# Performance work log

Hardware: AMD Instinct MI355X
Metric: run time of the kernel (lower is better)

## Reference

```python
import jax, jax.numpy as jnp
import numpy as np

HEADS = 8
DIM_HEAD = 64
SCALE = DIM_HEAD ** -0.5


def setup_inputs() -> dict:
    key = jax.random.key(0)
    ks = jax.random.split(key, 7)
    B, N, Dq = 2, 4096, 512
    M, Dc = 4096, 768
    inner = HEADS * DIM_HEAD  # 512
    x = jax.random.normal(ks[0], (B, N, Dq), dtype=jnp.float32)
    context = jax.random.normal(ks[1], (B, M, Dc), dtype=jnp.float32)
    # weights stored [in, out] (torch Linear weight transposed)
    Wq = jax.random.normal(ks[2], (Dq, inner), dtype=jnp.float32) * (Dq ** -0.5)
    Wk = jax.random.normal(ks[3], (Dc, inner), dtype=jnp.float32) * (Dc ** -0.5)
    Wv = jax.random.normal(ks[4], (Dc, inner), dtype=jnp.float32) * (Dc ** -0.5)
    Wo = jax.random.normal(ks[5], (inner, Dq), dtype=jnp.float32) * (inner ** -0.5)
    bo = jax.random.normal(ks[6], (Dq,), dtype=jnp.float32) * 0.01
    return {"x": x, "context": context, "Wq": Wq, "Wk": Wk, "Wv": Wv, "Wo": Wo, "bo": bo}


def reference(x, context, Wq, Wk, Wv, Wo, bo):
    B, N, _ = x.shape
    M = context.shape[1]
    h, d = HEADS, DIM_HEAD
    q = (x @ Wq).reshape(B, N, h, d)                      # b n h d
    k = ((context @ Wk) * SCALE).reshape(B, M, h, d)      # scale applied to k, as in source
    v = (context @ Wv).reshape(B, M, h, d)
    scores = jnp.einsum('bnhd,bmhd->bhnm', q, k)          # full QK^T
    attn = jax.nn.softmax(scores, axis=-1)
    out = jnp.einsum('bhnm,bmhd->bnhd', attn, v).reshape(B, N, h * d)
    return out @ Wo + bo  # dropout p=0.0 -> identity
```

## Files before the change

### kernel.cpp

```cpp
#include <hip/hip_runtime.h>

typedef unsigned short u16;
typedef __attribute__((ext_vector_type(4))) unsigned short u16x4;
typedef __attribute__((ext_vector_type(8))) unsigned short u16x8;
typedef __attribute__((ext_vector_type(8))) short s16x8;
typedef __attribute__((ext_vector_type(4))) float f32x4;
typedef __attribute__((ext_vector_type(16))) float f32x16;
typedef __attribute__((ext_vector_type(4))) unsigned int u32x4;

#define LOG2E 1.4426950408889634f

__device__ __forceinline__ u16 f2bf(float f) {
    return __builtin_bit_cast(unsigned short, static_cast<__bf16>(f));
}

__device__ __forceinline__ float bf2f(u16 v) {
    return __builtin_bit_cast(float, (unsigned)v << 16);
}

__device__ __forceinline__ float fexp2(float x) {
#if __has_builtin(__builtin_amdgcn_exp2f)
    return __builtin_amdgcn_exp2f(x);
#else
    return exp2f(x);
#endif
}

__device__ __forceinline__ s16x8 ld_frag(const u16* p) {
    return __builtin_bit_cast(s16x8, *reinterpret_cast<const u16x8*>(p));
}

__device__ __forceinline__ f32x4 mfma16(s16x8 a, s16x8 b, f32x4 c) {
    return __builtin_amdgcn_mfma_f32_16x16x32_bf16(a, b, c, 0, 0, 0);
}

__device__ __forceinline__ f32x16 mfma32(s16x8 a, s16x8 b, f32x16 c) {
    return __builtin_amdgcn_mfma_f32_32x32x16_bf16(a, b, c, 0, 0, 0);
}

__device__ __forceinline__ unsigned cvt_pk_bf16(float lo, float hi2) {
    unsigned r;
    asm("v_cvt_pk_bf16_f32 %0, %1, %2" : "=v"(r) : "v"(lo), "v"(hi2));
    return r;
}

__device__ __forceinline__ void plane32_swap(unsigned& x, unsigned& y) {
#if __has_builtin(__builtin_amdgcn_permlane32_swap)
    auto r = __builtin_amdgcn_permlane32_swap(x, y, false, false);
    x = r[0];
    y = r[1];
#else
    asm("v_permlane32_swap_b32 %0, %1" : "+v"(x), "+v"(y));
#endif
}

__device__ __forceinline__ void async16(const u16* g, u16* lds) {
    __builtin_amdgcn_global_load_lds(
        (__attribute__((address_space(1))) void*)const_cast<u16*>(g),
        (__attribute__((address_space(3))) void*)lds, 16, 0, 0);
}

__global__ __launch_bounds__(256) void prep_kernel(
    const float* __restrict__ x, const float* __restrict__ ctx, const float* __restrict__ Wq,
    const float* __restrict__ Wk, const float* __restrict__ Wv, const float* __restrict__ Wo,
    u16* __restrict__ xb, u16* __restrict__ cb, u16* __restrict__ Wqt, u16* __restrict__ Wkt,
    u16* __restrict__ Wvt, u16* __restrict__ Wot) {
    __shared__ float t[32][33];
    const int bidx = blockIdx.x;
    const int tid = threadIdx.x;
    if (bidx < 5120) {
        int i = bidx * 256 + tid;
        const float* in;
        u16* out;
        int idx;
        if (i < 524288) {
            in = x; out = xb; idx = i;
        } else {
            in = ctx; out = cb; idx = i - 524288;
        }
        const f32x4* p = (const f32x4*)in + ((size_t)idx << 1);
        f32x4 a = p[0], c = p[1];
        u16x8 v;
        v[0] = f2bf(a[0]); v[1] = f2bf(a[1]); v[2] = f2bf(a[2]); v[3] = f2bf(a[3]);
        v[4] = f2bf(c[0]); v[5] = f2bf(c[1]); v[6] = f2bf(c[2]); v[7] = f2bf(c[3]);
        *((u16x8*)out + idx) = v;
    } else {
        const int zb = bidx - 5120;
        const int z = zb / 384;
        const int rem = zb - z * 384;
        const int kx = rem % 24, ny = rem / 24;
        const float* W;
        u16* Wt;
        int Kd;
        float scale;
        switch (z) {
            case 0: W = Wq; Wt = Wqt; Kd = 512; scale = 1.0f; break;
            case 1: W = Wk; Wt = Wkt; Kd = 768; scale = 0.125f * LOG2E; break;
            case 2: W = Wv; Wt = Wvt; Kd = 768; scale = 1.0f; break;
            default: W = Wo; Wt = Wot; Kd = 512; scale = 1.0f; break;
        }
        const int k0 = kx << 5, n0 = ny << 5;
        if (k0 >= Kd) return;
        const int tx = tid & 31, ty = tid >> 5;
#pragma unroll
        for (int i = 0; i < 32; i += 8)
            t[ty + i][tx] = W[(size_t)(k0 + ty + i) * 512 + n0 + tx] * scale;
        __syncthreads();
#pragma unroll
        for (int i = 0; i < 32; i += 8)
            Wt[(size_t)(n0 + ty + i) * Kd + k0 + tx] = f2bf(t[tx][ty + i]);
    }
}

template <int MODE>
__device__ __forceinline__ void gemm_body(u16* __restrict__ Ab, u16* __restrict__ Bb,
                                          const u16* __restrict__ A, const u16* __restrict__ Bt,
                                          void* __restrict__ Cv, const float* __restrict__ bias,
                                          int K) {
    const int tid = threadIdx.x;
    const int w = tid >> 6, l = tid & 63;
    const int lg = l >> 4, lq = l & 15;
    const int wm = w >> 1, wn = w & 1;
    const int bm = blockIdx.y, bn = blockIdx.x;
    const int KT = K >> 6;

    f32x4 acc[4][4];
#pragma unroll
    for (int i = 0; i < 4; i++)
#pragma unroll
        for (int j = 0; j < 4; j++) acc[i][j] = (f32x4){0.f, 0.f, 0.f, 0.f};

    const u16* Ag0 = A + (size_t)bm * 128 * K;
    const u16* Bg0 = Bt + (size_t)bn * 128 * K;
    const int srow = l >> 3, scol = (l & 7) << 3;

    auto stage = [&](int kt, int buf) {
#pragma unroll
        for (int i = 0; i < 4; i++) {
            const int c = (w << 2) + i;
            const int row = (c << 3) + srow;
            async16(Ag0 + (size_t)row * K + kt * 64 + scol, Ab + (buf << 13) + (c << 9));
            async16(Bg0 + (size_t)row * K + kt * 64 + scol, Bb + (buf << 13) + (c << 9));
        }
    };

    stage(0, 0);
    for (int kt = 0; kt < KT; ++kt) {
        __syncthreads();
        if (kt + 1 < KT) stage(kt + 1, (kt + 1) & 1);
        const u16* As = Ab + ((kt & 1) << 13);
        const u16* Bs = Bb + ((kt & 1) << 13);
#pragma unroll
        for (int s = 0; s < 2; s++) {
            s16x8 af[4], bfr[4];
#pragma unroll
            for (int mt = 0; mt < 4; mt++)
                af[mt] = ld_frag(As + ((wm << 6) + (mt << 4) + lq) * 64 + (s << 5) + (lg << 3));
#pragma unroll
            for (int nt = 0; nt < 4; nt++)
                bfr[nt] = ld_frag(Bs + ((wn << 6) + (nt << 4) + lq) * 64 + (s << 5) + (lg << 3));
#pragma unroll
            for (int mt = 0; mt < 4; mt++)
#pragma unroll
                for (int nt = 0; nt < 4; nt++)
                    acc[mt][nt] = mfma16(af[mt], bfr[nt], acc[mt][nt]);
        }
    }
    const int row0 = bm * 128 + (wm << 6);
    const int col0 = bn * 128 + (wn << 6);
    if constexpr (MODE == 0) {
        u16* C = (u16*)Cv;
#pragma unroll
        for (int mt = 0; mt < 4; mt++)
#pragma unroll
            for (int nt = 0; nt < 4; nt++)
#pragma unroll
                for (int r = 0; r < 4; r++)
                    C[(size_t)(row0 + (mt << 4) + (lg << 2) + r) * 512 + col0 + (nt << 4) + lq] =
                        f2bf(acc[mt][nt][r]);
    } else if constexpr (MODE == 3) {
        float* C = (float*)Cv;
        float bv[4];
#pragma unroll
        for (int nt = 0; nt < 4; nt++) bv[nt] = bias[col0 + (nt << 4) + lq];
#pragma unroll
        for (int mt = 0; mt < 4; mt++)
#pragma unroll
            for (int nt = 0; nt < 4; nt++)
#pragma unroll
                for (int r = 0; r < 4; r++)
                    C[(size_t)(row0 + (mt << 4) + (lg << 2) + r) * 512 + col0 + (nt << 4) + lq] =
                        acc[mt][nt][r] + bv[nt];
    } else {
        __syncthreads();
        u16* Cl = Ab;
#pragma unroll
        for (int mt = 0; mt < 4; mt++)
#pragma unroll
            for (int nt = 0; nt < 4; nt++)
#pragma unroll
                for (int r = 0; r < 4; r++) {
                    const int m = row0 + (mt << 4) + (lg << 2) + r;
                    const int d = (col0 + (nt << 4) + lq) & 63;
                    const int kvl = m & 31;
                    const int tl = (m >> 5) & 3;
                    int op;
                    if constexpr (MODE == 1) {
                        op = ((d >> 4) << 9) + ((kvl + (((d >> 3) & 1) << 5)) << 3) + (d & 7);
                    } else {
                        const int lane = (d & 31) + (((kvl >> 3) & 1) << 5);
                        const int fi = ((kvl >> 4) << 1) + (d >> 5);
                        op = (fi << 9) + (lane << 3) + (kvl & 7);
                    }
                    Cl[(((wn << 2) + tl) << 11) + op] = f2bf(acc[mt][nt][r]);
                }
        __syncthreads();
        u16* C = (u16*)Cv;
#pragma unroll
        for (int c = 0; c < 8; c++) {
            const int bhc = ((bm >> 5) << 3) + (bn << 1) + (c >> 2);
            const int Tc = ((bm & 31) << 2) + (c & 3);
            u16* dst = C + ((size_t)((bhc << 7) + Tc) << 11);
            *(u16x8*)(dst + (tid << 3)) = *(const u16x8*)(Cl + (c << 11) + (tid << 3));
        }
    }
}

__global__ __launch_bounds__(256, 2) void proj_gemm_kernel(
    const u16* __restrict__ xb, const u16* __restrict__ cb, const u16* __restrict__ Wqt,
    const u16* __restrict__ Wkt, const u16* __restrict__ Wvt, u16* __restrict__ Qb,
    u16* __restrict__ Kp, u16* __restrict__ Vp) {
    __shared__ u16 Ab[2][8192];
    __shared__ u16 Bb[2][8192];
    const int z = blockIdx.z;
    if (z == 0)
        gemm_body<0>(&Ab[0][0], &Bb[0][0], xb, Wqt, Qb, nullptr, 512);
    else if (z == 1)
        gemm_body<1>(&Ab[0][0], &Bb[0][0], cb, Wkt, Kp, nullptr, 768);
    else
        gemm_body<2>(&Ab[0][0], &Bb[0][0], cb, Wvt, Vp, nullptr, 768);
}

__global__ __launch_bounds__(256, 2) void out_gemm_kernel(const u16* __restrict__ Ob,
                                                          const u16* __restrict__ Wot,
                                                          float* __restrict__ out,
                                                          const float* __restrict__ bias) {
    __shared__ u16 Ab[2][8192];
    __shared__ u16 Bb[2][8192];
    gemm_body<3>(&Ab[0][0], &Bb[0][0], Ob, Wot, out, bias, 512);
}

__global__ __launch_bounds__(256, 3) void attn_kernel(const u16* __restrict__ Qb,
                                                      const u16* __restrict__ Kp,
                                                      const u16* __restrict__ Vp,
                                                      u16* __restrict__ Opart,
                                                      float* __restrict__ Lpart) {
    __shared__ u16 Kl[2][4096];
    __shared__ u16 Vl[2][4096];
    const int tid = threadIdx.x;
    const int w = tid >> 6, l = tid & 63;
    const int lq = l & 31, hi = l >> 5;
    const int bid = blockIdx.x;
    const int swz = ((bid & 7) << 8) + (bid >> 3);
    const int bh = swz >> 7, qtg = (swz >> 2) & 31, kvseg = swz & 3;
    const int qt = (qtg << 2) + w;
    const int wid = (((bh << 7) + qt) << 2) + kvseg;
    const int b = bh >> 3, h = bh & 7;

    const u16* Qp = Qb + (size_t)(b * 4096 + (qt << 5) + lq) * 512 + (h << 6) + (hi << 3);
    s16x8 qf[4];
#pragma unroll
    for (int s = 0; s < 4; s++) qf[s] = ld_frag(Qp + (s << 4));

    const u16* Kg = Kp + ((size_t)(bh << 7) + (kvseg << 5)) * 2048;
    const u16* Vg = Vp + ((size_t)(bh << 7) + (kvseg << 5)) * 2048;
    const int gsrc = (w << 9) + (l << 3);
    const int ldst = w << 9;
    const int roff = l << 3;

    f32x16 oacc0 = {}, oacc1 = {};
    float rs = 0.f;

    async16(Kg + gsrc, &Kl[0][ldst]);
    async16(Kg + 2048 + gsrc, &Kl[0][2048 + ldst]);
    async16(Vg + gsrc, &Vl[0][ldst]);
    async16(Vg + 2048 + gsrc, &Vl[0][2048 + ldst]);

    auto qk = [&](const u16* Kb_) -> f32x16 {
        f32x16 sacc = {};
        s16x8 fa = ld_frag(Kb_ + roff);
        s16x8 fb = ld_frag(Kb_ + 512 + roff);
        __builtin_amdgcn_s_setprio(1);
        sacc = mfma32(fa, qf[0], sacc);
        fa = ld_frag(Kb_ + 1024 + roff);
        sacc = mfma32(fb, qf[1], sacc);
        fb = ld_frag(Kb_ + 1536 + roff);
        sacc = mfma32(fa, qf[2], sacc);
        sacc = mfma32(fb, qf[3], sacc);
        __builtin_amdgcn_s_setprio(0);
        return sacc;
    };

    auto softmax = [&](f32x16& sacc, s16x8 (&aw)[2]) {
#pragma unroll
        for (int r = 0; r < 16; r++) sacc[r] = fexp2(sacc[r]);
        {
            float t0 = (sacc[0] + sacc[1]) + (sacc[2] + sacc[3]);
            float t1 = (sacc[4] + sacc[5]) + (sacc[6] + sacc[7]);
            float t2 = (sacc[8] + sacc[9]) + (sacc[10] + sacc[11]);
            float t3 = (sacc[12] + sacc[13]) + (sacc[14] + sacc[15]);
            rs += (t0 + t1) + (t2 + t3);
        }
#pragma unroll
        for (int sp = 0; sp < 2; sp++) {
            const int base2 = sp << 3;
            unsigned X1 = cvt_pk_bf16(sacc[base2 + 0], sacc[base2 + 1]);
            unsigned Y1 = cvt_pk_bf16(sacc[base2 + 4], sacc[base2 + 5]);
            unsigned X2 = cvt_pk_bf16(sacc[base2 + 2], sacc[base2 + 3]);
            unsigned Y2 = cvt_pk_bf16(sacc[base2 + 6], sacc[base2 + 7]);
            plane32_swap(X1, Y1);
            plane32_swap(X2, Y2);
            u32x4 wv;
            wv[0] = X1; wv[1] = X2; wv[2] = Y1; wv[3] = Y2;
            aw[sp] = __builtin_bit_cast(s16x8, wv);
        }
    };

    auto pv = [&](const s16x8 (&aw)[2], const u16* Vb_) {
        s16x8 va = ld_frag(Vb_ + roff);
        s16x8 vb = ld_frag(Vb_ + 512 + roff);
        __builtin_amdgcn_s_setprio(1);
        oacc0 = mfma32(aw[0], va, oacc0);
        va = ld_frag(Vb_ + 1024 + roff);
        oacc1 = mfma32(aw[0], vb, oacc1);
        vb = ld_frag(Vb_ + 1536 + roff);
        oacc0 = mfma32(aw[1], va, oacc0);
        oacc1 = mfma32(aw[1], vb, oacc1);
        __builtin_amdgcn_s_setprio(0);
    };

    for (int t = 0; t < 16; ++t) {
        const int buf = t & 1;
        __syncthreads();
        if (t + 1 < 16) {
            const size_t base = (size_t)(t + 1) * 4096;
            const int nb = buf ^ 1;
            async16(Kg + base + gsrc, &Kl[nb][ldst]);
            async16(Kg + base + 2048 + gsrc, &Kl[nb][2048 + ldst]);
            async16(Vg + base + gsrc, &Vl[nb][ldst]);
            async16(Vg + base + 2048 + gsrc, &Vl[nb][2048 + ldst]);
        }
        f32x16 s0 = qk(&Kl[buf][0]);
        f32x16 s1 = qk(&Kl[buf][2048]);
        s16x8 aw0[2], aw1[2];
        softmax(s0, aw0);
        pv(aw0, &Vl[buf][0]);
        softmax(s1, aw1);
        pv(aw1, &Vl[buf][2048]);
    }

    u16* Ow = Opart + ((size_t)wid << 11);
#pragma unroll
    for (int r = 0; r < 16; r++) Ow[(r << 6) + l] = f2bf(oacc0[r]);
#pragma unroll
    for (int r = 0; r < 16; r++) Ow[((16 + r) << 6) + l] = f2bf(oacc1[r]);
    rs += __shfl_xor(rs, 32);
    if (l < 32) Lpart[(wid << 5) + l] = rs;
}

__global__ __launch_bounds__(256) void merge_kernel(const u16* __restrict__ Op,
                                                    const float* __restrict__ Lp,
                                                    u16* __restrict__ Ob) {
    const int g = blockIdx.x * 256 + threadIdx.x;
    const int slot = g >> 8;
    const int idx8 = (g & 255) << 3;
    const int dtr = idx8 >> 6;
    const int r = dtr & 15, dt = dtr >> 4;
    const int lane0 = idx8 & 63;
    const int q = (r & 3) + ((r >> 2) << 3) + ((lane0 >> 5) << 2);
    float lsum = 0.f;
#pragma unroll
    for (int p = 0; p < 4; p++) lsum += Lp[(slot << 7) + (p << 5) + q];
    const float ri = 1.f / lsum;
    float acc[8] = {0.f, 0.f, 0.f, 0.f, 0.f, 0.f, 0.f, 0.f};
#pragma unroll
    for (int p = 0; p < 4; p++) {
        const u16x8 a = *(const u16x8*)(Op + ((size_t)slot << 13) + (p << 11) + idx8);
#pragma unroll
        for (int j = 0; j < 8; j++) acc[j] += bf2f(a[j]);
    }
    u16x8 o;
#pragma unroll
    for (int j = 0; j < 8; j++) o[j] = f2bf(acc[j] * ri);
    const int bh = slot >> 7, qt = slot & 127;
    const int row = ((bh >> 3) << 12) + (qt << 5) + q;
    const int d = (lane0 & 31) + (dt << 5);
    *(u16x8*)(Ob + (size_t)row * 512 + ((bh & 7) << 6) + d) = o;
}

extern "C" void kernel_launch(void* const* d_in, const int* in_sizes, int n_in, void* d_out,
                              int out_size, void* d_ws, size_t ws_size, hipStream_t stream) {
    const float* x = (const float*)d_in[0];
    const float* ctx = (const float*)d_in[1];
    const float* Wq = (const float*)d_in[2];
    const float* Wk = (const float*)d_in[3];
    const float* Wv = (const float*)d_in[4];
    const float* Wo = (const float*)d_in[5];
    const float* bo = (const float*)d_in[6];
    float* out = (float*)d_out;

    char* ws = (char*)d_ws;
    u16* xb  = (u16*)(ws);
    u16* cb  = (u16*)(ws + 8388608);
    u16* Opart   = (u16*)(ws);
    float* Lpart = (float*)(ws + 33554432);
    u16* Qb  = (u16*)(ws + 34603008);
    u16* Ob  = (u16*)(ws + 34603008);
    u16* Kp  = (u16*)(ws + 42991616);
    u16* Vp  = (u16*)(ws + 51380224);
    u16* Wqt = (u16*)(ws + 59768832);
    u16* Wkt = (u16*)(ws + 60293120);
    u16* Wvt = (u16*)(ws + 61079552);
    u16* Wot = (u16*)(ws + 61865984);

    prep_kernel<<<dim3(6656), dim3(256), 0, stream>>>(x, ctx, Wq, Wk, Wv, Wo, xb, cb, Wqt, Wkt,
                                                      Wvt, Wot);
    proj_gemm_kernel<<<dim3(4, 64, 3), dim3(256), 0, stream>>>(xb, cb, Wqt, Wkt, Wvt, Qb, Kp, Vp);
    attn_kernel<<<dim3(2048), dim3(256), 0, stream>>>(Qb, Kp, Vp, Opart, Lpart);
    merge_kernel<<<dim3(2048), dim3(256), 0, stream>>>(Opart, Lpart, Ob);
    out_gemm_kernel<<<dim3(4, 64), dim3(256), 0, stream>>>(Ob, Wot, out, bo);
}
```

Before: 153.9 us.

## Fuse split-KV merge into output projection GEMM and drop setprio in attention

Removes the separate merge kernel and has the output-projection GEMM read the partial attention outputs and row sums directly. It combines the four KV segments, normalises, and writes the bf16 A tile into padded shared memory while the next B tile loads asynchronously. This drops one launch and a round trip of the merged O buffer through memory. The cost is that each of the 4 column blocks re-reads and re-merges the same partials, about four times the partial reads. It also removes the s_setprio hints around the MFMA groups in the attention kernel.

```diff
diff --git a/kernel.cpp b/kernel.cpp
--- a/kernel.cpp
+++ b/kernel.cpp
@@ -178,19 +178,6 @@
                 for (int r = 0; r < 4; r++)
                     C[(size_t)(row0 + (mt << 4) + (lg << 2) + r) * 512 + col0 + (nt << 4) + lq] =
                         f2bf(acc[mt][nt][r]);
-    } else if constexpr (MODE == 3) {
-        float* C = (float*)Cv;
-        float bv[4];
-#pragma unroll
-        for (int nt = 0; nt < 4; nt++) bv[nt] = bias[col0 + (nt << 4) + lq];
-#pragma unroll
-        for (int mt = 0; mt < 4; mt++)
-#pragma unroll
-            for (int nt = 0; nt < 4; nt++)
-#pragma unroll
-                for (int r = 0; r < 4; r++)
-                    C[(size_t)(row0 + (mt << 4) + (lg << 2) + r) * 512 + col0 + (nt << 4) + lq] =
-                        acc[mt][nt][r] + bv[nt];
     } else {
         __syncthreads();
         u16* Cl = Ab;
@@ -241,13 +228,119 @@
         gemm_body<2>(&Ab[0][0], &Bb[0][0], cb, Wvt, Vp, nullptr, 768);
 }
 
-__global__ __launch_bounds__(256, 2) void out_gemm_kernel(const u16* __restrict__ Ob,
-                                                          const u16* __restrict__ Wot,
-                                                          float* __restrict__ out,
-                                                          const float* __restrict__ bias) {
-    __shared__ u16 Ab[2][8192];
+__global__ __launch_bounds__(256, 2) void out_fused_kernel(
+    const u16* __restrict__ Op, const float* __restrict__ Lp, const u16* __restrict__ Wot,
+    float* __restrict__ out, const float* __restrict__ bias) {
+    __shared__ u16 As[2][128 * 72];
     __shared__ u16 Bb[2][8192];
-    gemm_body<3>(&Ab[0][0], &Bb[0][0], Ob, Wot, out, bias, 512);
+    const int tid = threadIdx.x;
+    const int w = tid >> 6, l = tid & 63;
+    const int lg = l >> 4, lq = l & 15;
+    const int wm = w >> 1, wn = w & 1;
+    const int bm = blockIdx.y, bn = blockIdx.x;
+    const int b = bm >> 5, qt0 = (bm & 31) << 2;
+
+    f32x4 acc[4][4];
+#pragma unroll
+    for (int i = 0; i < 4; i++)
+#pragma unroll
+        for (int j = 0; j < 4; j++) acc[i][j] = (f32x4){0.f, 0.f, 0.f, 0.f};
+
+    const u16* Bg0 = Wot + (size_t)bn * 128 * 512;
+    const int srow = l >> 3, scol = (l & 7) << 3;
+
+    auto stageB = [&](int kt, int buf) {
+#pragma unroll
+        for (int i = 0; i < 4; i++) {
+            const int c = (w << 2) + i;
+            const int row = (c << 3) + srow;
+            async16(Bg0 + (size_t)row * 512 + kt * 64 + scol, Bb[buf] + (c << 9));
+        }
+    };
+
+    u16x8 hA[4];
+    auto loadA = [&](int kt) {
+#pragma unroll
+        for (int c = 0; c < 4; c++) {
+            const int qtl = c;
+            const int rem = tid;
+            const int r = (rem >> 3) & 15;
+            const int j = rem & 7;
+            const int q32 = (r & 3) + ((r >> 2) << 3) + ((j >> 2) << 2);
+            const int slot = ((b << 3) + kt) * 128 + qt0 + qtl;
+            const u16* basep = Op + ((size_t)slot << 13) + (rem << 3);
+            float sum[8] = {0.f, 0.f, 0.f, 0.f, 0.f, 0.f, 0.f, 0.f};
+#pragma unroll
+            for (int p = 0; p < 4; p++) {
+                const u16x8 a = *(const u16x8*)(basep + (p << 11));
+#pragma unroll
+                for (int jj = 0; jj < 8; jj++) sum[jj] += bf2f(a[jj]);
+            }
+            const float ls = Lp[(slot << 7) + q32] + Lp[(slot << 7) + 32 + q32] +
+                             Lp[(slot << 7) + 64 + q32] + Lp[(slot << 7) + 96 + q32];
+            const float ri = 1.f / ls;
+            u16x8 hv;
+#pragma unroll
+            for (int jj = 0; jj < 8; jj++) hv[jj] = f2bf(sum[jj] * ri);
+            hA[c] = hv;
+        }
+    };
+    auto writeA = [&](int buf) {
+#pragma unroll
+        for (int c = 0; c < 4; c++) {
+            const int qtl = c;
+            const int rem = tid;
+            const int dt = rem >> 7;
+            const int r = (rem >> 3) & 15;
+            const int j = rem & 7;
+            const int q32 = (r & 3) + ((r >> 2) << 3) + ((j >> 2) << 2);
+            const int d0 = ((j & 3) << 3) + (dt << 5);
+            *(u16x8*)(&As[buf][((qtl << 5) + q32) * 72 + d0]) = hA[c];
+        }
+    };
+
+    stageB(0, 0);
+    loadA(0);
+    writeA(0);
+    for (int kt = 0; kt < 8; ++kt) {
+        __syncthreads();
+        const int buf = kt & 1;
+        if (kt + 1 < 8) {
+            stageB(kt + 1, buf ^ 1);
+            loadA(kt + 1);
+        }
+        const u16* Asb = As[buf];
+        const u16* Bs = Bb[buf];
+#pragma unroll
+        for (int s = 0; s < 2; s++) {
+            s16x8 af[4], bfr[4];
+#pragma unroll
+            for (int mt = 0; mt < 4; mt++)
+                af[mt] = ld_frag(Asb + ((wm << 6) + (mt << 4) + lq) * 72 + (s << 5) + (lg << 3));
+#pragma unroll
+            for (int nt = 0; nt < 4; nt++)
+                bfr[nt] = ld_frag(Bs + ((wn << 6) + (nt << 4) + lq) * 64 + (s << 5) + (lg << 3));
+#pragma unroll
+            for (int mt = 0; mt < 4; mt++)
+#pragma unroll
+                for (int nt = 0; nt < 4; nt++)
+                    acc[mt][nt] = mfma16(af[mt], bfr[nt], acc[mt][nt]);
+        }
+        if (kt + 1 < 8) writeA(buf ^ 1);
+    }
+    const int row0 = bm * 128 + (wm << 6);
+    const int col0 = bn * 128 + (wn << 6);
+    float bv[4];
+#pragma unroll
+    for (int nt = 0; nt < 4; nt++) bv[nt] = bias[col0 + (nt << 4) + lq];
+#pragma unroll
+    for (int mt = 0; mt < 4; mt++)
+#pragma unroll
+        for (int nt = 0; nt < 4; nt++)
+#pragma unroll
+            for (int r = 0; r < 4; r++)
+                out[(size_t)(row0 + (mt << 4) + (lg << 2) + r) * 512 + col0 + (nt << 4) + lq] =
+                    acc[mt][nt][r] + bv[nt];
 }
 
 __global__ __launch_bounds__(256, 3) void attn_kernel(const u16* __restrict__ Qb,
@@ -290,14 +383,12 @@
         f32x16 sacc = {};
         s16x8 fa = ld_frag(Kb_ + roff);
         s16x8 fb = ld_frag(Kb_ + 512 + roff);
-        __builtin_amdgcn_s_setprio(1);
         sacc = mfma32(fa, qf[0], sacc);
         fa = ld_frag(Kb_ + 1024 + roff);
         sacc = mfma32(fb, qf[1], sacc);
         fb = ld_frag(Kb_ + 1536 + roff);
         sacc = mfma32(fa, qf[2], sacc);
         sacc = mfma32(fb, qf[3], sacc);
-        __builtin_amdgcn_s_setprio(0);
         return sacc;
     };
 
@@ -329,14 +420,12 @@
     auto pv = [&](const s16x8 (&aw)[2], const u16* Vb_) {
         s16x8 va = ld_frag(Vb_ + roff);
         s16x8 vb = ld_frag(Vb_ + 512 + roff);
-        __builtin_amdgcn_s_setprio(1);
         oacc0 = mfma32(aw[0], va, oacc0);
         va = ld_frag(Vb_ + 1024 + roff);
         oacc1 = mfma32(aw[0], vb, oacc1);
         vb = ld_frag(Vb_ + 1536 + roff);
         oacc0 = mfma32(aw[1], va, oacc0);
         oacc1 = mfma32(aw[1], vb, oacc1);
-        __builtin_amdgcn_s_setprio(0);
     };
 
     for (int t = 0; t < 16; ++t) {
@@ -366,36 +455,6 @@
     for (int r = 0; r < 16; r++) Ow[((16 + r) << 6) + l] = f2bf(oacc1[r]);
     rs += __shfl_xor(rs, 32);
     if (l < 32) Lpart[(wid << 5) + l] = rs;
-}
-
-__global__ __launch_bounds__(256) void merge_kernel(const u16* __restrict__ Op,
-                                                    const float* __restrict__ Lp,
-                                                    u16* __restrict__ Ob) {
-    const int g = blockIdx.x * 256 + threadIdx.x;
-    const int slot = g >> 8;
-    const int idx8 = (g & 255) << 3;
-    const int dtr = idx8 >> 6;
-    const int r = dtr & 15, dt = dtr >> 4;
-    const int lane0 = idx8 & 63;
-    const int q = (r & 3) + ((r >> 2) << 3) + ((lane0 >> 5) << 2);
-    float lsum = 0.f;
-#pragma unroll
-    for (int p = 0; p < 4; p++) lsum += Lp[(slot << 7) + (p << 5) + q];
-    const float ri = 1.f / lsum;
-    float acc[8] = {0.f, 0.f, 0.f, 0.f, 0.f, 0.f, 0.f, 0.f};
-#pragma unroll
-    for (int p = 0; p < 4; p++) {
-        const u16x8 a = *(const u16x8*)(Op + ((size_t)slot << 13) + (p << 11) + idx8);
-#pragma unroll
-        for (int j = 0; j < 8; j++) acc[j] += bf2f(a[j]);
-    }
-    u16x8 o;
-#pragma unroll
-    for (int j = 0; j < 8; j++) o[j] = f2bf(acc[j] * ri);
-    const int bh = slot >> 7, qt = slot & 127;
-    const int row = ((bh >> 3) << 12) + (qt << 5) + q;
-    const int d = (lane0 & 31) + (dt << 5);
-    *(u16x8*)(Ob + (size_t)row * 512 + ((bh & 7) << 6) + d) = o;
 }
 
 extern "C" void kernel_launch(void* const* d_in, const int* in_sizes, int n_in, void* d_out,
@@ -415,7 +474,6 @@
     u16* Opart   = (u16*)(ws);
     float* Lpart = (float*)(ws + 33554432);
     u16* Qb  = (u16*)(ws + 34603008);
-    u16* Ob  = (u16*)(ws + 34603008);
     u16* Kp  = (u16*)(ws + 42991616);
     u16* Vp  = (u16*)(ws + 51380224);
     u16* Wqt = (u16*)(ws + 59768832);
@@ -427,6 +485,5 @@
                                                       Wvt, Wot);
     proj_gemm_kernel<<<dim3(4, 64, 3), dim3(256), 0, stream>>>(xb, cb, Wqt, Wkt, Wvt, Qb, Kp, Vp);
     attn_kernel<<<dim3(2048), dim3(256), 0, stream>>>(Qb, Kp, Vp, Opart, Lpart);
-    merge_kernel<<<dim3(2048), dim3(256), 0, stream>>>(Opart, Lpart, Ob);
-    out_gemm_kernel<<<dim3(4, 64), dim3(256), 0, stream>>>(Ob, Wot, out, bo);
-}
+    out_fused_kernel<<<dim3(4, 64), dim3(256), 0, stream>>>(Opart, Lpart, Wot, out, bo);
+}
```

New measurement: 160.8 us. 4.4% more time.
